# Performance work log

Measured on AMD Instinct MI355X. Metric: run time of the kernel, lower is better.

## Reference

```python
import jax, jax.numpy as jnp
import numpy as np

T, B, D = 64, 256, 2000
TN, E, H, A, V = 3000, 256, 256, 128, 128
PS, PE, S = 64, 64, 128
G1N, G1L, G2N, G2L = 1500, 4, 1500, 6


def setup_inputs():
    key = jax.random.key(0)
    ks = jax.random.split(key, 32)
    def nrm(k, shape, s=0.05):
        return jax.random.normal(k, shape, dtype=jnp.float32) * s
    inp = {}
    inp["X"] = jax.random.uniform(ks[0], (T, B, D), dtype=jnp.float32)
    inp["profiles"] = nrm(ks[1], (B, PS), 1.0)
    inp["ini_embd"] = nrm(ks[2], (TN, E), 1.0)
    inp["Wa_w"] = nrm(ks[3], (2 * E, A))
    inp["Wa_b"] = jnp.zeros((A,), jnp.float32)
    inp["Ua_w"] = nrm(ks[4], (A, 1))
    inp["gru_Wih"] = nrm(ks[5], (3 * H, E))
    inp["gru_Whh"] = nrm(ks[6], (3 * H, H))
    inp["gru_bih"] = jnp.zeros((3 * H,), jnp.float32)
    inp["gru_bhh"] = jnp.zeros((3 * H,), jnp.float32)
    inp["tranH_w"] = nrm(ks[7], (H + PE, E))
    inp["tranH_b"] = jnp.zeros((E,), jnp.float32)
    inp["out_w"] = nrm(ks[8], (H + V + PE, D))
    inp["out_b"] = jnp.zeros((D,), jnp.float32)
    inp["erase_w"] = nrm(ks[9], (E, V))
    inp["erase_b"] = jnp.zeros((V,), jnp.float32)
    inp["add_w"] = nrm(ks[10], (E, V))
    inp["add_b"] = jnp.zeros((V,), jnp.float32)
    inp["iniVam"] = nrm(ks[11], (S, V), 1.0)
    inp["emP_w"] = nrm(ks[12], (PS, PE))
    inp["emP_b"] = jnp.zeros((PE,), jnp.float32)
    inp["attnP_w"] = nrm(ks[13], (PE + V, PE))
    inp["attnP_b"] = jnp.zeros((PE,), jnp.float32)
    inp["KMIds"] = jax.random.randint(ks[14], (S,), 0, TN, dtype=jnp.int32)
    inp["leaves1"] = jax.random.randint(ks[15], (G1N, G1L), 0, TN, dtype=jnp.int32)
    inp["anc1"] = jax.random.randint(ks[16], (G1N, G1L), 0, TN, dtype=jnp.int32)
    inp["leaves2"] = jax.random.randint(ks[17], (G2N, G2L), 0, TN, dtype=jnp.int32)
    inp["anc2"] = jax.random.randint(ks[18], (G2N, G2L), 0, TN, dtype=jnp.int32)
    inp["mapInfo"] = jax.random.randint(ks[19], (D,), 0, G1N + G2N, dtype=jnp.int32)
    lens = jnp.sort(jax.random.randint(ks[20], (B,), 1, T + 1, dtype=jnp.int32))[::-1]
    inp["X_lengths"] = lens.at[0].set(T)
    return inp


def _forward(floats, ints):
    (X, profiles, ini_embd, Wa_w, Wa_b, Ua_w, gru_Wih, gru_Whh, gru_bih, gru_bhh,
     tranH_w, tranH_b, out_w, out_b, erase_w, erase_b, add_w, add_b, iniVam,
     emP_w, emP_b, attnP_w, attnP_b) = floats
    KMIds, leaves1, anc1, leaves2, anc2, mapInfo, X_lengths = ints

    # GRAM-style ontology attention over (leaf, ancestor) pairs, grouped by path length
    def group_embed(leaves, anc):
        le = ini_embd[leaves]                                     # [N,L,E]
        ae = ini_embd[anc]                                        # [N,L,E]
        hdn = jnp.tanh(jnp.concatenate([le, ae], axis=2) @ Wa_w + Wa_b)
        w = jax.nn.softmax(hdn @ Ua_w, axis=1)                    # [N,L,1]
        return jnp.sum(w * ae, axis=1)                            # [N,E]

    embedMat = jnp.concatenate([group_embed(leaves1, anc1),
                                group_embed(leaves2, anc2)], axis=0)[mapInfo]  # [D,E]
    Xe = jnp.einsum('tbd,de->tbe', X, embedMat)                   # [T,B,E]

    # packed-sequence GRU: frozen state / zero output beyond each sample's length
    mask = (jnp.arange(T)[:, None] < X_lengths[None, :])[..., None]  # [T,B,1]

    def gru_step(h, tup):
        x_t, m_t = tup
        gx = x_t @ gru_Wih.T + gru_bih
        gh = h @ gru_Whh.T + gru_bhh
        r = jax.nn.sigmoid(gx[:, :H] + gh[:, :H])
        z = jax.nn.sigmoid(gx[:, H:2 * H] + gh[:, H:2 * H])
        n = jnp.tanh(gx[:, 2 * H:] + r * gh[:, 2 * H:])
        h_new = (1.0 - z) * n + z * h
        h = jnp.where(m_t, h_new, h)
        return h, jnp.where(m_t, h, 0.0)

    h0 = jnp.zeros((B, H), jnp.float32)
    _, gru_out = jax.lax.scan(gru_step, h0, (Xe, mask))           # [T,B,H]

    prof = profiles @ emP_w + emP_b                               # [B,PE]
    prof_rep = jnp.broadcast_to(prof[None], (T, B, PE))
    tran = jnp.concatenate([gru_out, prof_rep], axis=2) @ tranH_w + tranH_b  # [T,B,E]
    KM = ini_embd[KMIds]                                          # [S,E]
    slot_w = jax.nn.softmax(jnp.einsum('tbe,se->tbs', tran, KM), axis=2)     # [T,B,S]

    # erase/add gates depend only on Xe -> precompute, then scan VM recurrence
    erase = jax.nn.sigmoid(Xe @ erase_w + erase_b)                # [T,B,V]
    add = jnp.tanh(Xe @ add_w + add_b)                            # [T,B,V]

    def mem_step(VM, tup):
        sw, er, ad = tup                                          # [B,S],[B,V],[B,V]
        read = jnp.einsum('bs,bsv->bv', sw, VM)
        VM = VM * (1.0 - sw[:, :, None] * er[:, None, :]) + sw[:, :, None] * ad[:, None, :]
        return VM, read

    VM0 = jnp.broadcast_to(iniVam[None], (B, S, V))
    _, read = jax.lax.scan(mem_step, VM0, (slot_w, erase, add))   # read: [T,B,V]

    attn = jax.nn.relu(jnp.concatenate([prof_rep, read], axis=2) @ attnP_w + attnP_b)
    prof2 = prof_rep * attn
    final = jnp.concatenate([gru_out, read, prof2], axis=2)       # [T,B,H+V+PE]
    # dropout is identity (eval / drop_rate=0)
    return jax.nn.softmax(final @ out_w + out_b, axis=2)          # [T,B,D]


def reference(X, profiles, ini_embd, Wa_w, Wa_b, Ua_w, gru_Wih, gru_Whh, gru_bih, gru_bhh, tranH_w, tranH_b, out_w, out_b, erase_w, erase_b, add_w, add_b, iniVam, emP_w, emP_b, attnP_w, attnP_b, KMIds, leaves1, anc1, leaves2, anc2, mapInfo, X_lengths):
    floats = (X, profiles, ini_embd, Wa_w, Wa_b, Ua_w, gru_Wih, gru_Whh, gru_bih, gru_bhh,
              tranH_w, tranH_b, out_w, out_b, erase_w, erase_b, add_w, add_b, iniVam,
              emP_w, emP_b, attnP_w, attnP_b)
    ints = (KMIds, leaves1, anc1, leaves2, anc2, mapInfo, X_lengths)
    return _forward(floats, ints)
```

## Files before the change

### kernel.cpp

```cpp
#include <hip/hip_runtime.h>
#include <hip/hip_bf16.h>
#include <cmath>

#define T_  64
#define B_  256
#define D_  2000
#define TN_ 3000
#define E_  256
#define H_  256
#define A_  128
#define V_  128
#define PS_ 64
#define PE_ 64
#define S_  128
#define G1N_ 1500
#define G1L_ 4
#define G2N_ 1500
#define G2L_ 6
#define M_  (T_ * B_)
#define KF_ (H_ + V_ + PE_)
#define NREG 28

typedef __attribute__((ext_vector_type(8))) short short8_t;
typedef __attribute__((ext_vector_type(4))) float floatx4;
typedef _Float16 __attribute__((ext_vector_type(2))) h2_t;
typedef _Float16 __attribute__((ext_vector_type(8))) h8_t;

static __device__ __forceinline__ float sigmoidf_(float x) {
    return 1.0f / (1.0f + __expf(-x));
}

static __device__ __forceinline__ void bsplit_(float v, __hip_bfloat16& hi, __hip_bfloat16& lo) {
    hi = __float2bfloat16(v);
    lo = __float2bfloat16(v - __bfloat162float(hi));
}

static __device__ __forceinline__ float dot2_(unsigned int w, unsigned int h, float acc) {
    union { unsigned int u; h2_t h; } cw, ch;
    cw.u = w; ch.u = h;
#if __has_builtin(__builtin_amdgcn_fdot2)
    return __builtin_amdgcn_fdot2(cw.h, ch.h, acc, false);
#else
    return acc + (float)cw.h[0] * (float)ch.h[0] + (float)cw.h[1] * (float)ch.h[1];
#endif
}

static __device__ __forceinline__ void gl_lds16(const void* g, void* l)
{
#if __has_builtin(__builtin_amdgcn_global_load_lds)
    __builtin_amdgcn_global_load_lds(
        (const __attribute__((address_space(1))) void*)g,
        (__attribute__((address_space(3))) void*)l, 16, 0, 0);
#else
    *(short8_t*)l = *(const short8_t*)g;
#endif
}

template<int DT>
static __device__ __forceinline__ floatx4 mfma16_(short8_t a, short8_t b, floatx4 c) {
    if constexpr (DT == 0) {
        return __builtin_amdgcn_mfma_f32_16x16x32_bf16(a, b, c, 0, 0, 0);
    } else {
        union { short8_t s; h8_t h; } ua, ub;
        ua.s = a; ub.s = b;
        return __builtin_amdgcn_mfma_f32_16x16x32_f16(ua.h, ub.h, c, 0, 0, 0);
    }
}

template<int EPI, bool ACCUM, int OUTMODE, int NPH, int DT>
__global__ __launch_bounds__(256)
void k_mgemm3(const __hip_bfloat16* __restrict__ Ahi, const __hip_bfloat16* __restrict__ Alo,
              const __hip_bfloat16* __restrict__ Bhi, const __hip_bfloat16* __restrict__ Blo,
              const float* __restrict__ bias, float* __restrict__ Cf,
              __hip_bfloat16* __restrict__ Chi, __hip_bfloat16* __restrict__ Clo,
              int K, int Nreal, int nblk)
{
    __shared__ __align__(16) short As[4096];
    __shared__ __align__(16) short Bs[4096];

    const int tid  = threadIdx.x;
    const int lane = tid & 63;
    const int w    = tid >> 6;
    const int wm   = w >> 1, wn = w & 1;
    const int lr   = lane & 15;
    const int lkc  = lane >> 4;

    const int bx = blockIdx.x;
    const int m0 = (bx / nblk) * 128;
    const int n0 = (bx % nblk) * 128;

    const int fa = 2 * w;
    const size_t aoff0 = (size_t)(m0 + fa * 16 + lr) * K + lkc * 8;
    const size_t aoff1 = aoff0 + (size_t)16 * K;
    const size_t boff0 = (size_t)(n0 + fa * 16 + lr) * K + lkc * 8;
    const size_t boff1 = boff0 + (size_t)16 * K;

    floatx4 acc[4][4];
#pragma unroll
    for (int i = 0; i < 4; ++i)
#pragma unroll
        for (int j = 0; j < 4; ++j) acc[i][j] = floatx4{0.f, 0.f, 0.f, 0.f};

#pragma unroll 1
    for (int ph = 0; ph < NPH; ++ph) {
        const __hip_bfloat16* Ap = (ph == 2) ? Alo : Ahi;
        const __hip_bfloat16* Bp = (ph == 1) ? Blo : Bhi;

#pragma unroll 1
        for (int k0 = 0; k0 < K; k0 += 32) {
            __syncthreads();
            gl_lds16(Ap + aoff0 + k0, &As[(fa    ) * 512 + lane * 8]);
            gl_lds16(Ap + aoff1 + k0, &As[(fa + 1) * 512 + lane * 8]);
            gl_lds16(Bp + boff0 + k0, &Bs[(fa    ) * 512 + lane * 8]);
            gl_lds16(Bp + boff1 + k0, &Bs[(fa + 1) * 512 + lane * 8]);
            __syncthreads();

            short8_t af[4], bf[4];
#pragma unroll
            for (int i = 0; i < 4; ++i)
                af[i] = *(const short8_t*)(const void*)&As[(wm * 4 + i) * 512 + lane * 8];
#pragma unroll
            for (int j = 0; j < 4; ++j)
                bf[j] = *(const short8_t*)(const void*)&Bs[(wn * 4 + j) * 512 + lane * 8];
#pragma unroll
            for (int i = 0; i < 4; ++i)
#pragma unroll
                for (int j = 0; j < 4; ++j)
                    acc[i][j] = mfma16_<DT>(af[i], bf[j], acc[i][j]);
        }
    }

#pragma unroll
    for (int i = 0; i < 4; ++i) {
        const int row = m0 + wm * 64 + i * 16 + (lane >> 4) * 4;
#pragma unroll
        for (int j = 0; j < 4; ++j) {
            const int col = n0 + wn * 64 + j * 16 + (lane & 15);
            if (col < Nreal) {
                float bv = bias ? bias[col] : 0.0f;
#pragma unroll
                for (int r = 0; r < 4; ++r) {
                    float v = acc[i][j][r] + bv;
                    if (EPI == 1) v = (col < 128) ? sigmoidf_(v) : tanhf(v);
                    if (EPI == 2) {
                        if (col < 128) v = sigmoidf_(v);
                        else if (col < 256) v = tanhf(v);
                    }
                    size_t o = (size_t)(row + r) * Nreal + col;
                    if (OUTMODE == 0) {
                        if (ACCUM) v += Cf[o];
                        Cf[o] = v;
                    } else if (OUTMODE == 1) {
                        __hip_bfloat16 h, l;
                        bsplit_(v, h, l);
                        Chi[o] = h; Clo[o] = l;
                    } else {
                        ((_Float16*)Chi)[o] = (_Float16)v;
                    }
                }
            }
        }
    }
}

__global__ __launch_bounds__(256)
void k_cvtX(const float* __restrict__ X, _Float16* __restrict__ XH)
{
    int idx = blockIdx.x * blockDim.x + threadIdx.x;
    if (idx >= M_ * 256) return;
    int m = idx >> 8, d0 = (idx & 255) * 8;
    _Float16 h[8];
    if (d0 + 7 < D_) {
        float4 p = *(const float4*)(X + (size_t)m * D_ + d0);
        float4 q = *(const float4*)(X + (size_t)m * D_ + d0 + 4);
        h[0]=(_Float16)p.x; h[1]=(_Float16)p.y; h[2]=(_Float16)p.z; h[3]=(_Float16)p.w;
        h[4]=(_Float16)q.x; h[5]=(_Float16)q.y; h[6]=(_Float16)q.z; h[7]=(_Float16)q.w;
    } else {
#pragma unroll
        for (int i = 0; i < 8; ++i)
            h[i] = (d0 + i < D_) ? (_Float16)X[(size_t)m * D_ + d0 + i] : (_Float16)0.0f;
    }
    *(short8_t*)(XH + (size_t)m * 2048 + d0) = *(short8_t*)h;
}

__global__ __launch_bounds__(256)
void k_mgemmXh(const _Float16* __restrict__ XH,
               const _Float16* __restrict__ Bhi, const _Float16* __restrict__ Blo,
               __hip_bfloat16* __restrict__ Chi, __hip_bfloat16* __restrict__ Clo)
{
    const int KP = 2048, NN = 256, nblk = 2;
    __shared__ __align__(16) short Ah[4096];
    __shared__ __align__(16) short Bh[4096];
    __shared__ __align__(16) short Bl[4096];

    const int tid  = threadIdx.x;
    const int lane = tid & 63;
    const int w    = tid >> 6;
    const int wm   = w >> 1, wn = w & 1;
    const int lr   = lane & 15;
    const int lkc  = lane >> 4;

    const int bx = blockIdx.x;
    const int m0 = (bx / nblk) * 128;
    const int n0 = (bx % nblk) * 128;

    const int fa = 2 * w;
    const size_t aoff0 = (size_t)(m0 + fa * 16 + lr) * KP + lkc * 8;
    const size_t aoff1 = aoff0 + (size_t)16 * KP;
    const size_t boff0 = (size_t)(n0 + fa * 16 + lr) * KP + lkc * 8;
    const size_t boff1 = boff0 + (size_t)16 * KP;

    floatx4 acc[4][4];
#pragma unroll
    for (int i = 0; i < 4; ++i)
#pragma unroll
        for (int j = 0; j < 4; ++j) acc[i][j] = floatx4{0.f, 0.f, 0.f, 0.f};

#pragma unroll 1
    for (int k0 = 0; k0 < KP; k0 += 32) {
        __syncthreads();
        gl_lds16(XH  + aoff0 + k0, &Ah[(fa    ) * 512 + lane * 8]);
        gl_lds16(XH  + aoff1 + k0, &Ah[(fa + 1) * 512 + lane * 8]);
        gl_lds16(Bhi + boff0 + k0, &Bh[(fa    ) * 512 + lane * 8]);
        gl_lds16(Bhi + boff1 + k0, &Bh[(fa + 1) * 512 + lane * 8]);
        gl_lds16(Blo + boff0 + k0, &Bl[(fa    ) * 512 + lane * 8]);
        gl_lds16(Blo + boff1 + k0, &Bl[(fa + 1) * 512 + lane * 8]);
        __syncthreads();

        short8_t af[4], bfh[4], bfl[4];
#pragma unroll
        for (int i = 0; i < 4; ++i) {
            af[i]  = *(const short8_t*)(const void*)&Ah[(wm * 4 + i) * 512 + lane * 8];
            bfh[i] = *(const short8_t*)(const void*)&Bh[(wn * 4 + i) * 512 + lane * 8];
        }
#pragma unroll
        for (int i = 0; i < 4; ++i)
#pragma unroll
            for (int j = 0; j < 4; ++j)
                acc[i][j] = mfma16_<1>(af[i], bfh[j], acc[i][j]);
#pragma unroll
        for (int j = 0; j < 4; ++j)
            bfl[j] = *(const short8_t*)(const void*)&Bl[(wn * 4 + j) * 512 + lane * 8];
#pragma unroll
        for (int i = 0; i < 4; ++i)
#pragma unroll
            for (int j = 0; j < 4; ++j)
                acc[i][j] = mfma16_<1>(af[i], bfl[j], acc[i][j]);
    }

#pragma unroll
    for (int i = 0; i < 4; ++i) {
        const int row = m0 + wm * 64 + i * 16 + (lane >> 4) * 4;
#pragma unroll
        for (int j = 0; j < 4; ++j) {
            const int col = n0 + wn * 64 + j * 16 + (lane & 15);
#pragma unroll
            for (int r = 0; r < 4; ++r) {
                float v = acc[i][j][r];
                size_t o = (size_t)(row + r) * NN + col;
                __hip_bfloat16 h, l;
                bsplit_(v, h, l);
                Chi[o] = h; Clo[o] = l;
            }
        }
    }
}

template<int BM, int BN, int BK, int TM, int TN>
__global__ __launch_bounds__(256)
void k_gemm(const float* __restrict__ A, const float* __restrict__ B,
            float* __restrict__ C, int M, int N, int K)
{
    __shared__ float As[BK][BM + 4];
    __shared__ float Bs[BK][BN + 4];
    const int tid = threadIdx.y * blockDim.x + threadIdx.x;
    const int m0 = blockIdx.y * BM;
    const int n0 = blockIdx.x * BN;
    float acc[TM][TN];
#pragma unroll
    for (int i = 0; i < TM; ++i)
#pragma unroll
        for (int j = 0; j < TN; ++j) acc[i][j] = 0.0f;
    for (int k0 = 0; k0 < K; k0 += BK) {
#pragma unroll
        for (int i = tid; i < BM * BK; i += 256) {
            int r = i / BK, c = i % BK;
            int m = m0 + r;
            As[c][r] = (m < M) ? A[(size_t)m * K + k0 + c] : 0.0f;
        }
#pragma unroll
        for (int i = tid; i < BK * BN; i += 256) {
            int r = i / BN, c = i % BN;
            Bs[r][c] = B[(size_t)(k0 + r) * N + n0 + c];
        }
        __syncthreads();
#pragma unroll
        for (int kk = 0; kk < BK; ++kk) {
            float a[TM], b[TN];
#pragma unroll
            for (int i = 0; i < TM; ++i) a[i] = As[kk][threadIdx.y * TM + i];
#pragma unroll
            for (int j = 0; j < TN; ++j) b[j] = Bs[kk][threadIdx.x * TN + j];
#pragma unroll
            for (int i = 0; i < TM; ++i)
#pragma unroll
                for (int j = 0; j < TN; ++j) acc[i][j] += a[i] * b[j];
        }
        __syncthreads();
    }
#pragma unroll
    for (int i = 0; i < TM; ++i) {
        int m = m0 + threadIdx.y * TM + i;
        if (m >= M) continue;
#pragma unroll
        for (int j = 0; j < TN; ++j)
            C[(size_t)m * N + n0 + threadIdx.x * TN + j] = acc[i][j];
    }
}

__global__ void k_pack_w2(const float* __restrict__ Wa_w, float* __restrict__ W2)
{
    int idx = blockIdx.x * blockDim.x + threadIdx.x;
    if (idx >= E_ * 2 * A_) return;
    int e = idx / (2 * A_), j = idx % (2 * A_);
    W2[idx] = (j < A_) ? Wa_w[(size_t)e * A_ + j]
                       : Wa_w[(size_t)(E_ + e) * A_ + (j - A_)];
}

__global__ void k_wg_split(const float* __restrict__ erase_w, const float* __restrict__ add_w,
                           const float* __restrict__ Wih,
                           const float* __restrict__ erase_b, const float* __restrict__ add_b,
                           const float* __restrict__ bih,
                           __hip_bfloat16* __restrict__ WGhi, __hip_bfloat16* __restrict__ WGlo,
                           float* __restrict__ biasG)
{
    int idx = blockIdx.x * blockDim.x + threadIdx.x;
    if (idx < 1024 * 256) {
        int n = idx >> 8, k = idx & 255;
        float v;
        if (n < 128)      v = erase_w[(size_t)k * V_ + n];
        else if (n < 256) v = add_w[(size_t)k * V_ + (n - 128)];
        else              v = Wih[(size_t)(n - 256) * 256 + k];
        bsplit_(v, WGhi[idx], WGlo[idx]);
    }
    if (idx < 1024)
        biasG[idx] = (idx < 128) ? erase_b[idx]
                   : (idx < 256) ? add_b[idx - 128]
                                 : bih[idx - 256];
}

__global__ void k_tranHT_split(const float* __restrict__ tranH_w,
                               __hip_bfloat16* __restrict__ hi, __hip_bfloat16* __restrict__ lo)
{
    int idx = blockIdx.x * blockDim.x + threadIdx.x;
    if (idx >= 256 * 320) return;
    int n = idx / 320, k = idx % 320;
    bsplit_(tranH_w[(size_t)k * 256 + n], hi[idx], lo[idx]);
}

__global__ void k_outWT_f16(const float* __restrict__ out_w, _Float16* __restrict__ dst)
{
    int idx = blockIdx.x * blockDim.x + threadIdx.x;
    if (idx >= 2048 * 448) return;
    int n = idx / 448, k = idx % 448;
    float v = (n < D_) ? out_w[(size_t)k * D_ + n] : 0.0f;
    dst[idx] = (_Float16)v;
}

__global__ void k_km_split(const float* __restrict__ ini_embd, const int* __restrict__ KMIds,
                           __hip_bfloat16* __restrict__ hi, __hip_bfloat16* __restrict__ lo)
{
    int idx = blockIdx.x * blockDim.x + threadIdx.x;
    if (idx >= S_ * E_) return;
    int s = idx / E_, k = idx % E_;
    bsplit_(ini_embd[(size_t)KMIds[s] * E_ + k], hi[idx], lo[idx]);
}

__global__ void k_embMT_f16(const float* __restrict__ embG, const int* __restrict__ mapInfo,
                            _Float16* __restrict__ hi, _Float16* __restrict__ lo)
{
    int idx = blockIdx.x * blockDim.x + threadIdx.x;
    if (idx >= 256 * 2048) return;
    int e = idx >> 11, d = idx & 2047;
    float v = (d < D_) ? embG[(size_t)mapInfo[d] * E_ + e] : 0.0f;
    _Float16 h = (_Float16)v;
    hi[idx] = h;
    lo[idx] = (_Float16)(v - (float)h);
}

__global__ void k_wgru_pack(const float* __restrict__ Whh,
                            unsigned int* __restrict__ Wrg, unsigned int* __restrict__ Wst)
{
    int idx = blockIdx.x * blockDim.x + threadIdx.x;
    if (idx >= 768 * 128) return;
    int j = idx / 128, e2 = idx % 128;
    union { unsigned int u; h2_t h; } c;
    c.h[0] = (_Float16)Whh[(size_t)j * 256 + 2 * e2];
    c.h[1] = (_Float16)Whh[(size_t)j * 256 + 2 * e2 + 1];
    if (e2 < 4 * NREG) {
        Wrg[(size_t)e2 * 768 + j] = c.u;
    } else {
        int ee = e2 - 4 * NREG;
        Wst[((size_t)(ee >> 2) * 768 + j) * 4 + (ee & 3)] = c.u;
    }
}

__global__ void k_prof(const float* __restrict__ profiles, const float* __restrict__ emP_w,
                       const float* __restrict__ emP_b, float* __restrict__ prof)
{
    int b = blockIdx.x, j = threadIdx.x;
    float acc = emP_b[j];
    for (int k = 0; k < PS_; ++k) acc += profiles[(size_t)b * PS_ + k] * emP_w[(size_t)k * PE_ + j];
    prof[(size_t)b * PE_ + j] = acc;
}

__global__ void k_fill_tp(const float* __restrict__ prof,
                          __hip_bfloat16* __restrict__ At_hi, __hip_bfloat16* __restrict__ At_lo)
{
    int idx = blockIdx.x * blockDim.x + threadIdx.x;
    if (idx >= M_ * PE_) return;
    int m = idx >> 6, pe = idx & 63;
    float v = prof[(size_t)(m & (B_ - 1)) * PE_ + pe];
    size_t o = (size_t)m * 320 + 256 + pe;
    bsplit_(v, At_hi[o], At_lo[o]);
}

__global__ void k_group_embed(const float* __restrict__ PP, const float* __restrict__ Wa_b,
                              const float* __restrict__ Ua_w, const float* __restrict__ ini_embd,
                              const int* __restrict__ leaves1, const int* __restrict__ anc1,
                              const int* __restrict__ leaves2, const int* __restrict__ anc2,
                              float* __restrict__ embedG)
{
    int n = blockIdx.x;
    int lane = threadIdx.x;
    const int* lv; const int* ac; int L;
    if (n < G1N_) { L = G1L_; lv = leaves1 + (size_t)n * G1L_; ac = anc1 + (size_t)n * G1L_; }
    else { int n2 = n - G1N_; L = G2L_; lv = leaves2 + (size_t)n2 * G2L_; ac = anc2 + (size_t)n2 * G2L_; }

    float score[6]; int ai[6];
    for (int l = 0; l < L; ++l) {
        int li = lv[l]; int av = ac[l]; ai[l] = av;
        float s = 0.0f;
        for (int a = lane; a < A_; a += 64) {
            float hv = tanhf(PP[(size_t)li * 256 + a] + PP[(size_t)av * 256 + 128 + a] + Wa_b[a]);
            s += hv * Ua_w[a];
        }
        for (int o = 32; o; o >>= 1) s += __shfl_xor(s, o);
        score[l] = s;
    }
    float mx = -1e30f;
    for (int l = 0; l < L; ++l) mx = fmaxf(mx, score[l]);
    float w[6], sum = 0.0f;
    for (int l = 0; l < L; ++l) { w[l] = __expf(score[l] - mx); sum += w[l]; }
    float inv = 1.0f / sum;
    for (int e = lane; e < E_; e += 64) {
        float acc = 0.0f;
        for (int l = 0; l < L; ++l) acc += w[l] * inv * ini_embd[(size_t)ai[l] * E_ + e];
        embedG[(size_t)n * E_ + e] = acc;
    }
}

__global__ __launch_bounds__(768, 3)
void k_gru5(const float* __restrict__ Cg, const unsigned int* __restrict__ Wrg,
            const uint4* __restrict__ Wst, const float* __restrict__ bhh,
            const int* __restrict__ X_len, float* __restrict__ gruo,
            __hip_bfloat16* __restrict__ At_hi, __hip_bfloat16* __restrict__ At_lo)
{
    const int b = blockIdx.x;
    const int tid = threadIdx.x;

    __shared__ uint4 h2S[32];
    __shared__ float ghS[768];
    __shared__ float gxnS[256];

    if (tid < 128) ((unsigned int*)h2S)[tid] = 0u;

    uint4 Wr[NREG];
#pragma unroll
    for (int c = 0; c < NREG; ++c) {
        Wr[c].x = Wrg[(size_t)(4 * c + 0) * 768 + tid];
        Wr[c].y = Wrg[(size_t)(4 * c + 1) * 768 + tid];
        Wr[c].z = Wrg[(size_t)(4 * c + 2) * 768 + tid];
        Wr[c].w = Wrg[(size_t)(4 * c + 3) * 768 + tid];
    }

    float hreg = 0.0f;
    const int len = X_len[b];
    const float bj = bhh[tid];
    __syncthreads();

    for (int t = 0; t < T_; ++t) {
        float gxv = Cg[((size_t)t * B_ + b) * 1024 + 256 + tid];

        float a0 = bj;
#pragma unroll
        for (int c = 0; c < 32; ++c) {
            uint4 w = (c < NREG) ? Wr[c] : Wst[(size_t)(c - NREG) * 768 + tid];
            uint4 h = h2S[c];
            a0 = dot2_(w.x, h.x, a0);
            a0 = dot2_(w.y, h.y, a0);
            a0 = dot2_(w.z, h.z, a0);
            a0 = dot2_(w.w, h.w, a0);
        }

        if (tid < 512) ghS[tid] = a0 + gxv;
        else { ghS[tid] = a0; gxnS[tid - 512] = gxv; }
        __syncthreads();

        if (tid < 256) {
            float r  = sigmoidf_(ghS[tid]);
            float z  = sigmoidf_(ghS[256 + tid]);
            float nn = tanhf(gxnS[tid] + r * ghS[512 + tid]);
            float hnew = (1.0f - z) * nn + z * hreg;
            bool msk = (t < len);
            hreg = msk ? hnew : hreg;
            float ov = msk ? hreg : 0.0f;
            size_t m = (size_t)t * B_ + b;
            gruo[m * H_ + tid] = ov;
            size_t o = m * 320 + tid;
            bsplit_(ov, At_hi[o], At_lo[o]);
            float partner = __shfl_xor(hreg, 1);
            if (!(tid & 1)) {
                union { unsigned int u; h2_t h; } p;
                p.h[0] = (_Float16)hreg;
                p.h[1] = (_Float16)partner;
                ((unsigned int*)h2S)[tid >> 1] = p.u;
            }
        }
        __syncthreads();
    }
}

__global__ __launch_bounds__(256)
void k_mem(const float* __restrict__ slotw, const float* __restrict__ Cg,
           const float* __restrict__ iniVam, float* __restrict__ readv)
{
    const int b = blockIdx.x;
    const int tid = threadIdx.x;
    const int v = tid & (V_ - 1);
    const int sh = tid >> 7;
    const int sbase = sh * 64;

    float VM[64];
#pragma unroll
    for (int i = 0; i < 64; ++i) VM[i] = iniVam[(size_t)(sbase + i) * V_ + v];

    __shared__ float swL[S_];
    __shared__ float eaL[2 * V_];
    __shared__ float part[V_];

    for (int t = 0; t < T_; ++t) {
        size_t m = (size_t)t * B_ + b;
        if (tid < S_) swL[tid] = slotw[m * S_ + tid];
        eaL[tid] = Cg[m * 1024 + tid];
        __syncthreads();

        float er = eaL[v], ad = eaL[V_ + v];
        float p0 = 0.0f, p1 = 0.0f, p2 = 0.0f, p3 = 0.0f;
#pragma unroll
        for (int i = 0; i < 16; ++i) {
            float s0 = swL[sbase + 4 * i];
            float s1 = swL[sbase + 4 * i + 1];
            float s2 = swL[sbase + 4 * i + 2];
            float s3 = swL[sbase + 4 * i + 3];
            float v0 = VM[4 * i], v1 = VM[4 * i + 1], v2 = VM[4 * i + 2], v3 = VM[4 * i + 3];
            p0 += s0 * v0; p1 += s1 * v1; p2 += s2 * v2; p3 += s3 * v3;
            VM[4 * i]     = v0 * (1.0f - s0 * er) + s0 * ad;
            VM[4 * i + 1] = v1 * (1.0f - s1 * er) + s1 * ad;
            VM[4 * i + 2] = v2 * (1.0f - s2 * er) + s2 * ad;
            VM[4 * i + 3] = v3 * (1.0f - s3 * er) + s3 * ad;
        }
        float acc = (p0 + p1) + (p2 + p3);
        if (sh == 1) part[v] = acc;
        __syncthreads();
        if (sh == 0) readv[m * V_ + v] = acc + part[v];
        __syncthreads();
    }
}

__global__ __launch_bounds__(256)
void k_build_final(const float* __restrict__ gruo, const float* __restrict__ readv,
                   const float* __restrict__ prof, const float* __restrict__ attnP_w,
                   const float* __restrict__ attnP_b, _Float16* __restrict__ F)
{
    const int m = blockIdx.x;
    const int b = m & (B_ - 1);
    const int tid = threadIdx.x;
    __shared__ float rd[V_];
    __shared__ float pf[PE_];
    if (tid < V_) rd[tid] = readv[(size_t)m * V_ + tid];
    if (tid < PE_) pf[tid] = prof[(size_t)b * PE_ + tid];
    __syncthreads();

    size_t base = (size_t)m * KF_;
    F[base + tid] = (_Float16)gruo[(size_t)m * H_ + tid];
    if (tid < V_) F[base + H_ + tid] = (_Float16)rd[tid];
    if (tid < PE_) {
        float a = attnP_b[tid];
        for (int k = 0; k < PE_; ++k) a += pf[k] * attnP_w[(size_t)k * PE_ + tid];
        for (int k = 0; k < V_; ++k) a += rd[k] * attnP_w[(size_t)(PE_ + k) * PE_ + tid];
        a = fmaxf(a, 0.0f);
        F[base + H_ + V_ + tid] = (_Float16)(pf[tid] * a);
    }
}

__global__ void k_softmax128(float* __restrict__ C)
{
    const int m = blockIdx.x;
    const size_t base = (size_t)m * S_;
    const int lane = threadIdx.x;
    float a = C[base + lane], b = C[base + 64 + lane];
    float mx = fmaxf(a, b);
    for (int o = 32; o; o >>= 1) mx = fmaxf(mx, __shfl_xor(mx, o));
    float e0 = __expf(a - mx), e1 = __expf(b - mx);
    float s = e0 + e1;
    for (int o = 32; o; o >>= 1) s += __shfl_xor(s, o);
    float inv = 1.0f / s;
    C[base + lane] = e0 * inv;
    C[base + 64 + lane] = e1 * inv;
}

__global__ __launch_bounds__(256)
void k_softmax2000(const _Float16* __restrict__ L, float* __restrict__ C)
{
    const int m = blockIdx.x;
    const size_t base = (size_t)m * D_;
    const int tid = threadIdx.x;
    const int wid = tid >> 6, lane = tid & 63;
    __shared__ float red[4], red2[4];

    float v[8];
#pragma unroll
    for (int i = 0; i < 8; ++i) {
        int d = i * 256 + tid;
        v[i] = (d < D_) ? (float)L[base + d] : -1e30f;
    }
    float mx = v[0];
#pragma unroll
    for (int i = 1; i < 8; ++i) mx = fmaxf(mx, v[i]);
    for (int o = 32; o; o >>= 1) mx = fmaxf(mx, __shfl_xor(mx, o));
    if (lane == 0) red[wid] = mx;
    __syncthreads();
    mx = fmaxf(fmaxf(red[0], red[1]), fmaxf(red[2], red[3]));

    float sum = 0.0f;
#pragma unroll
    for (int i = 0; i < 8; ++i) { v[i] = __expf(v[i] - mx); sum += v[i]; }
    for (int o = 32; o; o >>= 1) sum += __shfl_xor(sum, o);
    if (lane == 0) red2[wid] = sum;
    __syncthreads();
    sum = red2[0] + red2[1] + red2[2] + red2[3];
    float inv = 1.0f / sum;
#pragma unroll
    for (int i = 0; i < 8; ++i) {
        int d = i * 256 + tid;
        if (d < D_) C[base + d] = v[i] * inv;
    }
}

extern "C" void kernel_launch(void* const* d_in, const int* in_sizes, int n_in,
                              void* d_out, int out_size, void* d_ws, size_t ws_size,
                              hipStream_t stream)
{
    const float* X        = (const float*)d_in[0];
    const float* profiles = (const float*)d_in[1];
    const float* ini_embd = (const float*)d_in[2];
    const float* Wa_w     = (const float*)d_in[3];
    const float* Wa_b     = (const float*)d_in[4];
    const float* Ua_w     = (const float*)d_in[5];
    const float* gru_Wih  = (const float*)d_in[6];
    const float* gru_Whh  = (const float*)d_in[7];
    const float* gru_bih  = (const float*)d_in[8];
    const float* gru_bhh  = (const float*)d_in[9];
    const float* tranH_w  = (const float*)d_in[10];
    const float* tranH_b  = (const float*)d_in[11];
    const float* out_w    = (const float*)d_in[12];
    const float* out_b    = (const float*)d_in[13];
    const float* erase_w  = (const float*)d_in[14];
    const float* erase_b  = (const float*)d_in[15];
    const float* add_w    = (const float*)d_in[16];
    const float* add_b    = (const float*)d_in[17];
    const float* iniVam   = (const float*)d_in[18];
    const float* emP_w    = (const float*)d_in[19];
    const float* emP_b    = (const float*)d_in[20];
    const float* attnP_w  = (const float*)d_in[21];
    const float* attnP_b  = (const float*)d_in[22];
    const int* KMIds   = (const int*)d_in[23];
    const int* leaves1 = (const int*)d_in[24];
    const int* anc1    = (const int*)d_in[25];
    const int* leaves2 = (const int*)d_in[26];
    const int* anc2    = (const int*)d_in[27];
    const int* mapInfo = (const int*)d_in[28];
    const int* X_len   = (const int*)d_in[29];

    char* ws = (char*)d_ws;
    float* out = (float*)d_out;
    typedef __hip_bfloat16 bf16;

    const size_t R0 = 0;
    const size_t R1 = 67108864;
    const size_t R2 = 83886080;
    const size_t R3 = 100663296;
    size_t P = 121634816;
    const size_t EMBHI = P; P += 1048576;
    const size_t EMBLO = P; P += 1048576;
    const size_t OWF  = P; P += 1835008;
    const size_t WGHI = P; P += 524288;
    const size_t WGLO = P; P += 524288;
    const size_t THHI = P; P += 163840;
    const size_t THLO = P; P += 163840;
    const size_t KMHI = P; P += 65536;
    const size_t KMLO = P; P += 65536;
    const size_t WRG  = P; P += 344064;
    const size_t WST  = P; P += 49152;
    const size_t PROF = P; P += 65536;
    const size_t BIAS = P; P += 4096;
    const size_t W2O  = P; P += 262144;

    float* PP      = (float*)(ws + R0);
    float* embG    = (float*)(ws + R0 + 12288000);
    _Float16* XH   = (_Float16*)(ws + R0);
    float* Cg      = (float*)(ws + R0);
    _Float16* F16  = (_Float16*)(ws + R0);
    _Float16* LG16 = (_Float16*)(ws + 16777216);
    float* gruo    = (float*)(ws + R1);
    bf16*  Xe_hi   = (bf16*)(ws + R2);
    bf16*  Xe_lo   = (bf16*)(ws + R2 + 8388608);
    bf16*  tran_hi = (bf16*)(ws + R2);
    bf16*  tran_lo = (bf16*)(ws + R2 + 8388608);
    bf16*  At_hi   = (bf16*)(ws + R3);
    bf16*  At_lo   = (bf16*)(ws + R3 + 10485760);
    float* slotw   = (float*)(ws + R3);
    float* readv   = (float*)(ws + R3 + 10485760);
    _Float16* EMBhi = (_Float16*)(ws + EMBHI);
    _Float16* EMBlo = (_Float16*)(ws + EMBLO);
    _Float16* OWf = (_Float16*)(ws + OWF);
    bf16*  WGhi = (bf16*)(ws + WGHI); bf16* WGlo = (bf16*)(ws + WGLO);
    bf16*  THhi = (bf16*)(ws + THHI); bf16* THlo = (bf16*)(ws + THLO);
    bf16*  KMhi = (bf16*)(ws + KMHI); bf16* KMlo = (bf16*)(ws + KMLO);
    unsigned int* Wrg = (unsigned int*)(ws + WRG);
    unsigned int* Wst = (unsigned int*)(ws + WST);
    float* prof  = (float*)(ws + PROF);
    float* biasG = (float*)(ws + BIAS);
    float* W2p   = (float*)(ws + W2O);

    k_pack_w2<<<(E_ * 2 * A_ + 255) / 256, 256, 0, stream>>>(Wa_w, W2p);
    k_wg_split<<<(1024 * 256 + 255) / 256, 256, 0, stream>>>(
        erase_w, add_w, gru_Wih, erase_b, add_b, gru_bih, WGhi, WGlo, biasG);
    k_tranHT_split<<<(256 * 320 + 255) / 256, 256, 0, stream>>>(tranH_w, THhi, THlo);
    k_outWT_f16<<<(2048 * 448 + 255) / 256, 256, 0, stream>>>(out_w, OWf);
    k_km_split<<<(S_ * E_ + 255) / 256, 256, 0, stream>>>(ini_embd, KMIds, KMhi, KMlo);
    k_wgru_pack<<<(768 * 128 + 255) / 256, 256, 0, stream>>>(gru_Whh, Wrg, Wst);
    k_prof<<<B_, PE_, 0, stream>>>(profiles, emP_w, emP_b, prof);

    {
        dim3 blk(16, 16);
        dim3 grid(4, (TN_ + 63) / 64);
        k_gemm<64, 64, 16, 4, 4><<<grid, blk, 0, stream>>>(ini_embd, W2p, PP, TN_, 256, E_);
    }
    k_group_embed<<<G1N_ + G2N_, 64, 0, stream>>>(PP, Wa_b, Ua_w, ini_embd,
                                                  leaves1, anc1, leaves2, anc2, embG);
    k_embMT_f16<<<(256 * 2048) / 256, 256, 0, stream>>>(embG, mapInfo, EMBhi, EMBlo);

    k_cvtX<<<(M_ * 256) / 256, 256, 0, stream>>>(X, XH);

    k_mgemmXh<<<128 * 2, 256, 0, stream>>>(XH, EMBhi, EMBlo, Xe_hi, Xe_lo);

    k_mgemm3<2, false, 0, 3, 0><<<128 * 8, 256, 0, stream>>>(Xe_hi, Xe_lo, WGhi, WGlo,
        biasG, Cg, nullptr, nullptr, 256, 1024, 8);

    k_gru5<<<256, 768, 0, stream>>>(Cg, Wrg, (const uint4*)Wst, gru_bhh, X_len,
                                    gruo, At_hi, At_lo);
    k_fill_tp<<<(M_ * PE_) / 256, 256, 0, stream>>>(prof, At_hi, At_lo);

    k_mgemm3<0, false, 1, 3, 0><<<128 * 2, 256, 0, stream>>>(At_hi, At_lo, THhi, THlo,
        tranH_b, nullptr, tran_hi, tran_lo, 320, 256, 2);

    k_mgemm3<0, false, 0, 3, 0><<<128 * 1, 256, 0, stream>>>(tran_hi, tran_lo, KMhi, KMlo,
        nullptr, slotw, nullptr, nullptr, 256, 128, 1);

    k_softmax128<<<M_, 64, 0, stream>>>(slotw);
    k_mem<<<B_, 256, 0, stream>>>(slotw, Cg, iniVam, readv);
    k_build_final<<<M_, 256, 0, stream>>>(gruo, readv, prof, attnP_w, attnP_b, F16);

    k_mgemm3<0, false, 2, 1, 1><<<128 * 16, 256, 0, stream>>>(
        (const bf16*)F16, nullptr, (const bf16*)OWf, nullptr,
        out_b, nullptr, (bf16*)LG16, nullptr, 448, 2000, 16);

    k_softmax2000<<<M_, 256, 0, stream>>>(LG16, out);
}
```

Baseline: 691.5 us.

## Double-buffer LDS tiles in MFMA GEMMs and remap blocks per XCD

Both MFMA GEMM kernels now keep two LDS buffers, so the global-to-LDS copy of the next K tile is issued before the MFMAs on the current tile, with one barrier per iteration instead of two. Block indices are also remapped so that consecutive M tiles land on the same XCD, which is meant to improve L2 reuse of the shared B operand. The cost is twice the LDS footprint, which may lower occupancy, and the remap assumes the grid size divides evenly by 8*nblk.

```diff
diff --git a/kernel.cpp b/kernel.cpp
--- a/kernel.cpp
+++ b/kernel.cpp
@@ -75,8 +75,8 @@
               __hip_bfloat16* __restrict__ Chi, __hip_bfloat16* __restrict__ Clo,
               int K, int Nreal, int nblk)
 {
-    __shared__ __align__(16) short As[4096];
-    __shared__ __align__(16) short Bs[4096];
+    __shared__ __align__(16) short As[2][4096];
+    __shared__ __align__(16) short Bs[2][4096];
 
     const int tid  = threadIdx.x;
     const int lane = tid & 63;
@@ -86,8 +86,10 @@
     const int lkc  = lane >> 4;
 
     const int bx = blockIdx.x;
-    const int m0 = (bx / nblk) * 128;
-    const int n0 = (bx % nblk) * 128;
+    const int xcd = bx & 7, loc = bx >> 3;
+    const int mchunk = (int)gridDim.x / (8 * nblk);
+    const int m0 = (xcd * mchunk + loc / nblk) * 128;
+    const int n0 = (loc % nblk) * 128;
 
     const int fa = 2 * w;
     const size_t aoff0 = (size_t)(m0 + fa * 16 + lr) * K + lkc * 8;
@@ -95,39 +97,52 @@
     const size_t boff0 = (size_t)(n0 + fa * 16 + lr) * K + lkc * 8;
     const size_t boff1 = boff0 + (size_t)16 * K;
 
+    const int lA0 = (fa    ) * 512 + lane * 8;
+    const int lA1 = (fa + 1) * 512 + lane * 8;
+
     floatx4 acc[4][4];
 #pragma unroll
     for (int i = 0; i < 4; ++i)
 #pragma unroll
         for (int j = 0; j < 4; ++j) acc[i][j] = floatx4{0.f, 0.f, 0.f, 0.f};
 
+    const int KT = K >> 5;
+    const int NT = NPH * KT;
+
+    int s_ph = 0, s_k = 0;
+    auto do_stage = [&](int buf) {
+        const __hip_bfloat16* Ap = (s_ph == 2) ? Alo : Ahi;
+        const __hip_bfloat16* Bp = (s_ph == 1) ? Blo : Bhi;
+        gl_lds16(Ap + aoff0 + s_k, &As[buf][lA0]);
+        gl_lds16(Ap + aoff1 + s_k, &As[buf][lA1]);
+        gl_lds16(Bp + boff0 + s_k, &Bs[buf][lA0]);
+        gl_lds16(Bp + boff1 + s_k, &Bs[buf][lA1]);
+        s_k += 32;
+        if (s_k >= K) { s_k = 0; ++s_ph; }
+    };
+
+    do_stage(0);
+    __syncthreads();
+
 #pragma unroll 1
-    for (int ph = 0; ph < NPH; ++ph) {
-        const __hip_bfloat16* Ap = (ph == 2) ? Alo : Ahi;
-        const __hip_bfloat16* Bp = (ph == 1) ? Blo : Bhi;
-
-#pragma unroll 1
-        for (int k0 = 0; k0 < K; k0 += 32) {
-            __syncthreads();
-            gl_lds16(Ap + aoff0 + k0, &As[(fa    ) * 512 + lane * 8]);
-            gl_lds16(Ap + aoff1 + k0, &As[(fa + 1) * 512 + lane * 8]);
-            gl_lds16(Bp + boff0 + k0, &Bs[(fa    ) * 512 + lane * 8]);
-            gl_lds16(Bp + boff1 + k0, &Bs[(fa + 1) * 512 + lane * 8]);
-            __syncthreads();
-
-            short8_t af[4], bf[4];
-#pragma unroll
-            for (int i = 0; i < 4; ++i)
-                af[i] = *(const short8_t*)(const void*)&As[(wm * 4 + i) * 512 + lane * 8];
+    for (int t = 0; t < NT; ++t) {
+        const int cur = t & 1;
+        if (t + 1 < NT) do_stage(cur ^ 1);
+
+        short8_t af[4], bf[4];
+#pragma unroll
+        for (int i = 0; i < 4; ++i)
+            af[i] = *(const short8_t*)(const void*)&As[cur][(wm * 4 + i) * 512 + lane * 8];
+#pragma unroll
+        for (int j = 0; j < 4; ++j)
+            bf[j] = *(const short8_t*)(const void*)&Bs[cur][(wn * 4 + j) * 512 + lane * 8];
+#pragma unroll
+        for (int i = 0; i < 4; ++i)
 #pragma unroll
             for (int j = 0; j < 4; ++j)
-                bf[j] = *(const short8_t*)(const void*)&Bs[(wn * 4 + j) * 512 + lane * 8];
-#pragma unroll
-            for (int i = 0; i < 4; ++i)
-#pragma unroll
-                for (int j = 0; j < 4; ++j)
-                    acc[i][j] = mfma16_<DT>(af[i], bf[j], acc[i][j]);
-        }
+                acc[i][j] = mfma16_<DT>(af[i], bf[j], acc[i][j]);
+
+        __syncthreads();
     }
 
 #pragma unroll
@@ -189,9 +204,9 @@
                __hip_bfloat16* __restrict__ Chi, __hip_bfloat16* __restrict__ Clo)
 {
     const int KP = 2048, NN = 256, nblk = 2;
-    __shared__ __align__(16) short Ah[4096];
-    __shared__ __align__(16) short Bh[4096];
-    __shared__ __align__(16) short Bl[4096];
+    __shared__ __align__(16) short Ah[2][4096];
+    __shared__ __align__(16) short Bh[2][4096];
+    __shared__ __align__(16) short Bl[2][4096];
 
     const int tid  = threadIdx.x;
     const int lane = tid & 63;
@@ -201,8 +216,10 @@
     const int lkc  = lane >> 4;
 
     const int bx = blockIdx.x;
-    const int m0 = (bx / nblk) * 128;
-    const int n0 = (bx % nblk) * 128;
+    const int xcd = bx & 7, loc = bx >> 3;
+    const int mchunk = 256 / (8 * nblk);
+    const int m0 = (xcd * mchunk + loc / nblk) * 128;
+    const int n0 = (loc % nblk) * 128;
 
     const int fa = 2 * w;
     const size_t aoff0 = (size_t)(m0 + fa * 16 + lr) * KP + lkc * 8;
@@ -210,28 +227,39 @@
     const size_t boff0 = (size_t)(n0 + fa * 16 + lr) * KP + lkc * 8;
     const size_t boff1 = boff0 + (size_t)16 * KP;
 
+    const int lA0 = (fa    ) * 512 + lane * 8;
+    const int lA1 = (fa + 1) * 512 + lane * 8;
+
     floatx4 acc[4][4];
 #pragma unroll
     for (int i = 0; i < 4; ++i)
 #pragma unroll
         for (int j = 0; j < 4; ++j) acc[i][j] = floatx4{0.f, 0.f, 0.f, 0.f};
 
+    int s_k = 0;
+    auto do_stage = [&](int buf) {
+        gl_lds16(XH  + aoff0 + s_k, &Ah[buf][lA0]);
+        gl_lds16(XH  + aoff1 + s_k, &Ah[buf][lA1]);
+        gl_lds16(Bhi + boff0 + s_k, &Bh[buf][lA0]);
+        gl_lds16(Bhi + boff1 + s_k, &Bh[buf][lA1]);
+        gl_lds16(Blo + boff0 + s_k, &Bl[buf][lA0]);
+        gl_lds16(Blo + boff1 + s_k, &Bl[buf][lA1]);
+        s_k += 32;
+    };
+
+    do_stage(0);
+    __syncthreads();
+
 #pragma unroll 1
-    for (int k0 = 0; k0 < KP; k0 += 32) {
-        __syncthreads();
-        gl_lds16(XH  + aoff0 + k0, &Ah[(fa    ) * 512 + lane * 8]);
-        gl_lds16(XH  + aoff1 + k0, &Ah[(fa + 1) * 512 + lane * 8]);
-        gl_lds16(Bhi + boff0 + k0, &Bh[(fa    ) * 512 + lane * 8]);
-        gl_lds16(Bhi + boff1 + k0, &Bh[(fa + 1) * 512 + lane * 8]);
-        gl_lds16(Blo + boff0 + k0, &Bl[(fa    ) * 512 + lane * 8]);
-        gl_lds16(Blo + boff1 + k0, &Bl[(fa + 1) * 512 + lane * 8]);
-        __syncthreads();
+    for (int t = 0; t < KP / 32; ++t) {
+        const int cur = t & 1;
+        if (s_k < KP) do_stage(cur ^ 1);
 
         short8_t af[4], bfh[4], bfl[4];
 #pragma unroll
         for (int i = 0; i < 4; ++i) {
-            af[i]  = *(const short8_t*)(const void*)&Ah[(wm * 4 + i) * 512 + lane * 8];
-            bfh[i] = *(const short8_t*)(const void*)&Bh[(wn * 4 + i) * 512 + lane * 8];
+            af[i]  = *(const short8_t*)(const void*)&Ah[cur][(wm * 4 + i) * 512 + lane * 8];
+            bfh[i] = *(const short8_t*)(const void*)&Bh[cur][(wn * 4 + i) * 512 + lane * 8];
         }
 #pragma unroll
         for (int i = 0; i < 4; ++i)
@@ -240,12 +268,14 @@
                 acc[i][j] = mfma16_<1>(af[i], bfh[j], acc[i][j]);
 #pragma unroll
         for (int j = 0; j < 4; ++j)
-            bfl[j] = *(const short8_t*)(const void*)&Bl[(wn * 4 + j) * 512 + lane * 8];
+            bfl[j] = *(const short8_t*)(const void*)&Bl[cur][(wn * 4 + j) * 512 + lane * 8];
 #pragma unroll
         for (int i = 0; i < 4; ++i)
 #pragma unroll
             for (int j = 0; j < 4; ++j)
                 acc[i][j] = mfma16_<1>(af[i], bfl[j], acc[i][j]);
+
+        __syncthreads();
     }
 
 #pragma unroll
```

New measurement: 671.6 us. 1.03x faster.
